# Performance work log

Measured on AMD Instinct MI355X. Metric: run time of the kernel, lower is better.

Reference implementation:

```python
import jax, jax.numpy as jnp
import numpy as np

H = 2048
EPS = 1e-12

def setup_inputs() -> dict:
    key = jax.random.key(0)
    ks = jax.random.split(key, 12)
    B, S = 2, 4096
    scale = 1.0 / np.sqrt(H)
    inp = {
        "hidden_states": jax.random.normal(ks[0], (B, S, H), dtype=jnp.float32),
        "token_type_ids": jax.random.randint(ks[1], (B, S), 0, 2, dtype=jnp.int32),
        "ln_gamma": jnp.ones((H,), jnp.float32),
        "ln_beta": jnp.zeros((H,), jnp.float32),
        "tw1": jax.random.uniform(ks[2], (H, H), jnp.float32, -scale, scale),
        "tb1": jnp.zeros((H,), jnp.float32),
        "tw2": jax.random.uniform(ks[3], (H, H), jnp.float32, -scale, scale),
        "tb2": jnp.zeros((H,), jnp.float32),
        "iw1": jax.random.uniform(ks[4], (H, H), jnp.float32, -scale, scale),
        "ib1": jnp.zeros((H,), jnp.float32),
        "iw2": jax.random.uniform(ks[5], (H, H), jnp.float32, -scale, scale),
        "ib2": jnp.zeros((H,), jnp.float32),
    }
    return inp

def _layernorm(x, g, b):
    mu = jnp.mean(x, axis=-1, keepdims=True)
    var = jnp.mean(jnp.square(x - mu), axis=-1, keepdims=True)
    return (x - mu) * jax.lax.rsqrt(var + EPS) * g + b

def _mlp(x, w1, b1, w2, b2):
    # Linear -> exact GELU -> Linear (torch nn.GELU default is erf-based)
    h = jax.nn.gelu(jnp.einsum('bsh,hk->bsk', x, w1) + b1, approximate=False)
    return jnp.einsum('bsk,kh->bsh', h, w2) + b2

def reference(hidden_states, token_type_ids, ln_gamma, ln_beta,
              tw1, tb1, tw2, tb2, iw1, ib1, iw2, ib2):
    xn = _layernorm(hidden_states, ln_gamma, ln_beta)
    text_mask = (token_type_ids == 0)[..., None]   # [B,S,1]
    image_mask = (token_type_ids == 1)[..., None]
    text_out = _mlp(xn, tw1, tb1, tw2, tb2) * text_mask
    image_out = _mlp(xn, iw1, ib1, iw2, ib2) * image_mask
    # dropout is identity in inference / p=0
    return hidden_states + text_out + image_out
```

## Files before the change

kernel.cpp:

```cpp
#include <hip/hip_runtime.h>
#include <hip/hip_bf16.h>


#define H_DIM 2048
#define FULLROWS 8192
#define TAILROWS 512
#define KSPLIT 8

typedef __attribute__((ext_vector_type(8))) short s16x8;
typedef __attribute__((ext_vector_type(4))) float f32x4;
typedef __attribute__((ext_vector_type(4))) int   i32x4;

typedef __attribute__((address_space(1))) const unsigned int gu32;
typedef __attribute__((address_space(3))) unsigned int lu32;
typedef __attribute__((address_space(3))) short lds_s;

__device__ __forceinline__ void load_lds16(const void* g, void* l) {
  __builtin_amdgcn_global_load_lds((gu32*)g, (lu32*)l, 16, 0, 0);
}

__device__ __forceinline__ s16x8 asbf(i32x4 v) {
  union { i32x4 i; s16x8 s; } u; u.i = v; return u.s;
}

__global__ __launch_bounds__(256) void partition_kernel(
    const int* __restrict__ tt, int T, int* __restrict__ ctrl,
    int* __restrict__ pos, int* __restrict__ rowid) {
  __shared__ int psum[256];
  const int tid = threadIdx.x;
  const int npt = T >> 8;
  const int base = tid * npt;
  int cnt = 0;
  for (int i = 0; i < npt; ++i) cnt += (tt[base + i] == 0);
  psum[tid] = cnt;
  __syncthreads();
  for (int off = 1; off < 256; off <<= 1) {
    int v = psum[tid];
    int add = (tid >= off) ? psum[tid - off] : 0;
    __syncthreads();
    psum[tid] = v + add;
    __syncthreads();
  }
  const int Mt = psum[255];
  const int Mt_pad = (Mt + 255) & ~255;
  int tpos = psum[tid] - cnt;
  int ipos = base - tpos;
  for (int i = 0; i < npt; ++i) {
    const int tok = base + i;
    int p;
    if (tt[tok] == 0) p = tpos++;
    else              p = Mt_pad + ipos++;
    pos[tok] = p;
    rowid[p] = tok;
  }
  const int Mi = T - Mt;
  const int Mi_pad = (Mi + 255) & ~255;
  for (int g = Mt + tid; g < Mt_pad; g += 256) rowid[g] = -1;
  for (int g = Mt_pad + Mi + tid; g < Mt_pad + Mi_pad; g += 256) rowid[g] = -1;
  for (int g = Mt_pad + Mi_pad + tid; g < FULLROWS + TAILROWS; g += 256)
    rowid[g] = -1;
  if (tid == 0) {
    ctrl[0] = Mt; ctrl[1] = Mt_pad; ctrl[2] = Mi; ctrl[3] = Mi_pad;
    ctrl[4] = Mt_pad + Mi_pad;
  }
}

__global__ __launch_bounds__(256) void pad_zero_kernel(
    const int* __restrict__ ctrl, __hip_bfloat16* __restrict__ XG) {
  const int Mt = ctrl[0], Mt_pad = ctrl[1], Mi = ctrl[2];
  const int n1 = Mt_pad - Mt;
  const int start2 = Mt_pad + Mi;
  const int b = blockIdx.x;
  int row;
  if (b < n1) row = Mt + b;
  else {
    const int b2 = b - n1;
    if (start2 + b2 >= FULLROWS + TAILROWS) return;
    row = start2 + b2;
  }
  const int4 z = {0, 0, 0, 0};
  *(int4*)(XG + (size_t)row * H_DIM + threadIdx.x * 8) = z;
}

__global__ __launch_bounds__(256) void transpose_to_bf16(
    const float* __restrict__ W, __hip_bfloat16* __restrict__ WT) {
  __shared__ float tile[32][33];
  const int bx = blockIdx.x, by = blockIdx.y;
  const int tid = threadIdx.x;
  const int r = tid >> 3, c4 = (tid & 7) * 4;
  const float4 v = *(const float4*)(W + (size_t)(by * 32 + r) * H_DIM + bx * 32 + c4);
  tile[r][c4 + 0] = v.x; tile[r][c4 + 1] = v.y;
  tile[r][c4 + 2] = v.z; tile[r][c4 + 3] = v.w;
  __syncthreads();
  union { ushort u[4]; ushort4 v4; } pk;
#pragma unroll
  for (int j = 0; j < 4; ++j) {
    __hip_bfloat16 h = __float2bfloat16(tile[c4 + j][r]);
    pk.u[j] = *(const ushort*)&h;
  }
  *(ushort4*)(WT + (size_t)(bx * 32 + r) * H_DIM + by * 32 + c4) = pk.v4;
}

__global__ __launch_bounds__(256) void ln_scatter_kernel(
    const float* __restrict__ X, const float* __restrict__ gamma,
    const float* __restrict__ beta, const int* __restrict__ pos,
    __hip_bfloat16* __restrict__ XG) {
  const int t = blockIdx.x, tid = threadIdx.x;
  const float* row = X + (size_t)t * H_DIM;
  float x[8];
  {
    float4 v0 = *(const float4*)(row + tid * 8);
    float4 v1 = *(const float4*)(row + tid * 8 + 4);
    x[0] = v0.x; x[1] = v0.y; x[2] = v0.z; x[3] = v0.w;
    x[4] = v1.x; x[5] = v1.y; x[6] = v1.z; x[7] = v1.w;
  }
  float s = 0.f, q = 0.f;
#pragma unroll
  for (int j = 0; j < 8; ++j) { s += x[j]; q += x[j] * x[j]; }
#pragma unroll
  for (int off = 32; off > 0; off >>= 1) {
    s += __shfl_down(s, off);
    q += __shfl_down(q, off);
  }
  __shared__ float ls[4], lq[4];
  if ((tid & 63) == 0) { ls[tid >> 6] = s; lq[tid >> 6] = q; }
  __syncthreads();
  const float S = ls[0] + ls[1] + ls[2] + ls[3];
  const float Q = lq[0] + lq[1] + lq[2] + lq[3];
  const float mu = S * (1.0f / H_DIM);
  const float var = Q * (1.0f / H_DIM) - mu * mu;
  const float rstd = rsqrtf(var + 1e-12f);
  const int p = pos[t];
  float4 g0 = *(const float4*)(gamma + tid * 8);
  float4 g1 = *(const float4*)(gamma + tid * 8 + 4);
  float4 b0 = *(const float4*)(beta + tid * 8);
  float4 b1 = *(const float4*)(beta + tid * 8 + 4);
  float g[8] = {g0.x, g0.y, g0.z, g0.w, g1.x, g1.y, g1.z, g1.w};
  float b[8] = {b0.x, b0.y, b0.z, b0.w, b1.x, b1.y, b1.z, b1.w};
  union { ushort u[8]; int4 v; } pk;
#pragma unroll
  for (int j = 0; j < 8; ++j) {
    float y = (x[j] - mu) * rstd * g[j] + b[j];
    __hip_bfloat16 h = __float2bfloat16(y);
    pk.u[j] = *(const ushort*)&h;
  }
  *(int4*)(XG + (size_t)p * H_DIM + tid * 8) = pk.v;
}

#define DSRD(dst, addr, OFF) \
  asm volatile("ds_read_b128 %0, %1 offset:" OFF : "=v"(dst) : "v"(addr))
#define PBAR asm volatile("s_barrier" ::: "memory")
#define SB0  __builtin_amdgcn_sched_barrier(0)
#define LGKM0 do { \
  asm volatile("s_waitcnt lgkmcnt(0)" ::: "memory"); SB0; } while (0)
#define VM0 asm volatile("s_waitcnt vmcnt(0)" ::: "memory")

__device__ __forceinline__ float gelu_exact(float z) {
  return 0.5f * z * (1.0f + erff(z * 0.70710678118654752f));
}

template <int EPI>
__global__ __launch_bounds__(512, 2) void gemmk(
    const __hip_bfloat16* __restrict__ A,
    const __hip_bfloat16* __restrict__ WTt, const __hip_bfloat16* __restrict__ WTi,
    const float* __restrict__ bt, const float* __restrict__ bi,
    const int* __restrict__ ctrl, const int* __restrict__ rowid,
    __hip_bfloat16* __restrict__ Hout,
    const float* __restrict__ resid, float* __restrict__ Out,
    float* __restrict__ pp) {
  constexpr int K = H_DIM;
  const int Mt_pad = ctrl[1];

  __shared__ __align__(16) char smem[131072];
  const unsigned sBase = (unsigned)(uintptr_t)(lds_s*)smem;

  const int tid = threadIdx.x;
  const int w = tid >> 6, l = tid & 63;
  const int bid = blockIdx.x;

  const int srow8 = l >> 3;
  const int sg = (l & 7) ^ srow8;
  const int r16 = l & 15;
  const int r4base = (l >> 4) * 4;
  const int hl = (l & 15) >> 1;
  const int gr = (((l & 1) << 2) | (l >> 4)) ^ hl;

  if (bid < 256) {
    constexpr int NT = K / 64;
    const int m0 = (bid >> 3) * 256;
    const int n0 = (bid & 7) * 256;
    const bool is_text = (m0 < Mt_pad);
    const short* Ag = (const short*)A;
    const short* Bg = (const short*)(is_text ? WTt : WTi);
    const float* bias = is_text ? bt : bi;

    const int wm = w >> 2, wn = w & 3;
    const int scol8 = sg * 8;

    auto stageA = [&](int bI, int h, int kk) {
#pragma unroll
      for (int c = 0; c < 2; ++c) {
        const short* src = Ag + (size_t)(m0 + h * 128 + c * 64 + w * 8 + srow8) * K + kk + scol8;
        load_lds16(src, smem + bI * 32768 + h * 16384 + (c * 4096 + w * 512) * 2);
      }
    };
    auto stageB = [&](int bI, int h, int kk) {
#pragma unroll
      for (int c = 0; c < 2; ++c) {
        const short* src = Bg + (size_t)(n0 + h * 128 + c * 64 + w * 8 + srow8) * K + kk + scol8;
        load_lds16(src, smem + 65536 + bI * 32768 + h * 16384 + (c * 4096 + w * 512) * 2);
      }
    };

    int off2[2];
#pragma unroll
    for (int ks = 0; ks < 2; ++ks)
      off2[ks] = r16 * 64 + (((ks * 4 + (l >> 4)) ^ (l & 7)) * 8);

    unsigned ardA[2][2], ardB[2][2];
#pragma unroll
    for (int bI = 0; bI < 2; ++bI)
#pragma unroll
      for (int ks = 0; ks < 2; ++ks) {
        ardA[bI][ks] = sBase + bI * 32768u + (unsigned)(wm * 16384 + off2[ks] * 2);
        ardB[bI][ks] = sBase + 65536u + bI * 32768u +
                       (unsigned)((wn >> 1) * 16384 + ((wn & 1) * 4096 + off2[ks]) * 2);
      }

    i32x4 a[4][2], b[4][2];
    f32x4 acc[8][4];
    const f32x4 zero = {0.f, 0.f, 0.f, 0.f};
#pragma unroll
    for (int i = 0; i < 8; ++i)
#pragma unroll
      for (int j = 0; j < 4; ++j) acc[i][j] = zero;

    auto mfmaQ = [&](int fmBase, int fnBase) {
#pragma unroll
      for (int fm = 0; fm < 4; ++fm)
#pragma unroll
        for (int fn = 0; fn < 2; ++fn)
#pragma unroll
          for (int ks = 0; ks < 2; ++ks)
            acc[fmBase + fm][fnBase + fn] = __builtin_amdgcn_mfma_f32_16x16x32_bf16(
                asbf(a[fm][ks]), asbf(b[fnBase + fn][ks]),
                acc[fmBase + fm][fnBase + fn], 0, 0, 0);
    };

#define TILE(C) do {                                                          \
    DSRD(a[0][0], ardA[C][0], "0");     DSRD(a[0][1], ardA[C][1], "0");       \
    DSRD(a[1][0], ardA[C][0], "2048");  DSRD(a[1][1], ardA[C][1], "2048");    \
    DSRD(a[2][0], ardA[C][0], "4096");  DSRD(a[2][1], ardA[C][1], "4096");    \
    DSRD(a[3][0], ardA[C][0], "6144");  DSRD(a[3][1], ardA[C][1], "6144");    \
    DSRD(b[0][0], ardB[C][0], "0");     DSRD(b[0][1], ardB[C][1], "0");       \
    DSRD(b[1][0], ardB[C][0], "2048");  DSRD(b[1][1], ardB[C][1], "2048");    \
    stageA(C ^ 1, 0, _kA);                                                    \
    PBAR; LGKM0;                                                              \
    __builtin_amdgcn_s_setprio(1); mfmaQ(0, 0); __builtin_amdgcn_s_setprio(0);\
    SB0; PBAR;                                                                \
    DSRD(b[2][0], ardB[C][0], "4096");  DSRD(b[2][1], ardB[C][1], "4096");    \
    DSRD(b[3][0], ardB[C][0], "6144");  DSRD(b[3][1], ardB[C][1], "6144");    \
    stageA(C ^ 1, 1, _kA);                                                    \
    PBAR; LGKM0;                                                              \
    __builtin_amdgcn_s_setprio(1); mfmaQ(0, 2); __builtin_amdgcn_s_setprio(0);\
    SB0; PBAR;                                                                \
    DSRD(a[0][0], ardA[C][0], "8192");  DSRD(a[0][1], ardA[C][1], "8192");    \
    DSRD(a[1][0], ardA[C][0], "10240"); DSRD(a[1][1], ardA[C][1], "10240");   \
    DSRD(a[2][0], ardA[C][0], "12288"); DSRD(a[2][1], ardA[C][1], "12288");   \
    DSRD(a[3][0], ardA[C][0], "14336"); DSRD(a[3][1], ardA[C][1], "14336");   \
    stageB(C, 0, _kB);                                                        \
    PBAR; LGKM0;                                                              \
    __builtin_amdgcn_s_setprio(1); mfmaQ(4, 2); __builtin_amdgcn_s_setprio(0);\
    SB0; PBAR;                                                                \
    stageB(C, 1, _kB);                                                        \
    asm volatile("s_waitcnt vmcnt(4)" ::: "memory");                          \
    PBAR; SB0;                                                                \
    __builtin_amdgcn_s_setprio(1); mfmaQ(4, 0); __builtin_amdgcn_s_setprio(0);\
    SB0; PBAR;                                                                \
  } while (0)

    stageA(0, 0, 0); stageA(0, 1, 0);
    stageB(0, 0, 0); stageB(0, 1, 0);
    stageB(1, 0, 64); stageB(1, 1, 64);
    asm volatile("s_waitcnt vmcnt(4)" ::: "memory");
    PBAR;

    int _kA, _kB;
    for (int t = 0; t < NT; t += 2) {
      _kA = (t + 1 < NT ? t + 1 : NT - 1) * 64;
      _kB = (t + 2 < NT ? t + 2 : NT - 1) * 64;
      TILE(0);
      _kA = (t + 2 < NT ? t + 2 : NT - 1) * 64;
      _kB = (t + 3 < NT ? t + 3 : NT - 1) * 64;
      TILE(1);
    }
#undef TILE
    asm volatile("s_waitcnt vmcnt(0) lgkmcnt(0)" ::: "memory");

    float bb[4];
#pragma unroll
    for (int fn = 0; fn < 4; ++fn) bb[fn] = bias[n0 + wn * 64 + fn * 16 + r16];
    if (EPI == 0) {
#pragma unroll
      for (int fm = 0; fm < 8; ++fm) {
        const int grow = m0 + wm * 128 + fm * 16 + r4base;
#pragma unroll
        for (int fn = 0; fn < 4; ++fn) {
          const int gcol = n0 + wn * 64 + fn * 16 + r16;
          f32x4 v = acc[fm][fn];
#pragma unroll
          for (int i = 0; i < 4; ++i)
            Hout[(size_t)(grow + i) * K + gcol] = __float2bfloat16(gelu_exact(v[i] + bb[fn]));
        }
      }
    } else {
#pragma unroll
      for (int fm = 0; fm < 8; ++fm) {
        const int grow = m0 + wm * 128 + fm * 16 + r4base;
        int rid[4];
#pragma unroll
        for (int i = 0; i < 4; ++i) rid[i] = rowid[grow + i];
#pragma unroll
        for (int fn = 0; fn < 4; ++fn) {
          const int gcol = n0 + wn * 64 + fn * 16 + r16;
          f32x4 v = acc[fm][fn];
#pragma unroll
          for (int i = 0; i < 4; ++i) {
            if (rid[i] >= 0) {
              const size_t o = (size_t)rid[i] * K + gcol;
              Out[o] = resid[o] + v[i] + bb[fn];
            }
          }
        }
      }
    }
  } else {
    const int tb = bid - 256;
    const int kp = tb & 7;
    const int n0 = ((tb >> 3) & 7) * 256;
    const int m0 = FULLROWS + (tb >> 6) * 128;
    const int kk0 = kp * 256;
    const bool is_text = (m0 < Mt_pad);
    const short* Ag = (const short*)A;
    const short* Bg = (const short*)(is_text ? WTt : WTi);

    const int wm = w >> 2, wn = w & 3;
    const int sRowAdj = sg >> 2;
    const int sKAdj = (sg & 3) * 8;

    auto stageA = [&](int bI, int kk) {
      const int mr = w * 8 + srow8;
      const short* src = Ag + (size_t)(m0 + mr * 2 + sRowAdj) * K + kk + sKAdj;
      load_lds16(src, smem + bI * 8192 + w * 1024);
    };
    auto stageB = [&](int bI, int c2, int kk) {
      const int mr = c2 * 64 + w * 8 + srow8;
      const short* src = Bg + (size_t)(n0 + mr * 2 + sRowAdj) * K + kk + sKAdj;
      load_lds16(src, smem + 16384 + bI * 16384 + c2 * 8192 + w * 1024);
    };

    unsigned ardA[2], ardB[2];
#pragma unroll
    for (int bI = 0; bI < 2; ++bI) {
      ardA[bI] = sBase + bI * 8192u + (unsigned)(wm * 4096 + hl * 128 + gr * 16);
      ardB[bI] = sBase + 16384u + bI * 16384u + (unsigned)(wn * 4096 + hl * 128 + gr * 16);
    }

    i32x4 a[4], b[4];
    f32x4 acc[4][4];
    const f32x4 zero = {0.f, 0.f, 0.f, 0.f};
#pragma unroll
    for (int i = 0; i < 4; ++i)
#pragma unroll
      for (int j = 0; j < 4; ++j) acc[i][j] = zero;

#define RD_TILE(C) do {                                                   \
    DSRD(a[0], ardA[C], "0");    DSRD(a[1], ardA[C], "1024");             \
    DSRD(a[2], ardA[C], "2048"); DSRD(a[3], ardA[C], "3072");             \
    DSRD(b[0], ardB[C], "0");    DSRD(b[1], ardB[C], "1024");             \
    DSRD(b[2], ardB[C], "2048"); DSRD(b[3], ardB[C], "3072");             \
  } while (0)

    stageA(0, kk0);
    stageB(0, 0, kk0); stageB(0, 1, kk0);
    VM0;
    PBAR;

    for (int i = 0; i < 8; ++i) {
      const int c = i & 1;
      const int kn = kk0 + (i + 1 < 8 ? i + 1 : 7) * 32;
      stageA(c ^ 1, kn);
      stageB(c ^ 1, 0, kn); stageB(c ^ 1, 1, kn);
      RD_TILE(c);
      LGKM0;
      __builtin_amdgcn_s_setprio(1);
#pragma unroll
      for (int f = 0; f < 4; ++f)
#pragma unroll
        for (int fn = 0; fn < 4; ++fn)
          acc[f][fn] = __builtin_amdgcn_mfma_f32_16x16x32_bf16(
              asbf(a[f]), asbf(b[fn]), acc[f][fn], 0, 0, 0);
      __builtin_amdgcn_s_setprio(0);
      SB0;
      VM0;
      PBAR;
    }
#undef RD_TILE
    asm volatile("s_waitcnt vmcnt(0) lgkmcnt(0)" ::: "memory");

    float* ppk = pp + (size_t)kp * TAILROWS * H_DIM;
    const int mrel = m0 - FULLROWS;
#pragma unroll
    for (int fm = 0; fm < 4; ++fm) {
      const int prow = mrel + wm * 64 + fm * 16 + r4base;
#pragma unroll
      for (int fn = 0; fn < 4; ++fn) {
        const int gcol = n0 + wn * 64 + fn * 16 + r16;
        f32x4 v = acc[fm][fn];
#pragma unroll
        for (int i = 0; i < 4; ++i)
          ppk[(size_t)(prow + i) * H_DIM + gcol] = v[i];
      }
    }
  }
}

template <int EPI>
__global__ __launch_bounds__(256) void combine_kernel(
    const float* __restrict__ pp, const float* __restrict__ bt,
    const float* __restrict__ bi, const int* __restrict__ ctrl,
    const int* __restrict__ rowid, __hip_bfloat16* __restrict__ Hout,
    const float* __restrict__ resid, float* __restrict__ Out) {
  const int u = blockIdx.x * 256 + threadIdx.x;
  const int r = u >> 9;
  const int c = (u & 511) * 4;
  const size_t off = (size_t)r * H_DIM + c;
  float4 s = *(const float4*)(pp + off);
#pragma unroll
  for (int k = 1; k < KSPLIT; ++k) {
    const float4 sk = *(const float4*)(pp + (size_t)k * TAILROWS * H_DIM + off);
    s.x += sk.x; s.y += sk.y; s.z += sk.z; s.w += sk.w;
  }
  const int grow = FULLROWS + r;
  const float* bias = (grow < ctrl[1]) ? bt : bi;
  const float4 bb = *(const float4*)(bias + c);
  if (EPI == 0) {
    union { ushort u4[4]; ushort4 v4; } pk;
    float z[4] = {s.x + bb.x, s.y + bb.y, s.z + bb.z, s.w + bb.w};
#pragma unroll
    for (int j = 0; j < 4; ++j) {
      __hip_bfloat16 h = __float2bfloat16(0.5f * z[j] * (1.0f + erff(z[j] * 0.70710678118654752f)));
      pk.u4[j] = *(const ushort*)&h;
    }
    *(ushort4*)(Hout + (size_t)grow * H_DIM + c) = pk.v4;
  } else {
    const int rid = rowid[grow];
    if (rid >= 0) {
      const size_t o = (size_t)rid * H_DIM + c;
      const float4 rv = *(const float4*)(resid + o);
      float4 ov;
      ov.x = rv.x + s.x + bb.x; ov.y = rv.y + s.y + bb.y;
      ov.z = rv.z + s.z + bb.z; ov.w = rv.w + s.w + bb.w;
      *(float4*)(Out + o) = ov;
    }
  }
}

extern "C" void kernel_launch(void* const* d_in, const int* in_sizes, int n_in,
                              void* d_out, int out_size, void* d_ws, size_t ws_size,
                              hipStream_t stream) {
  const float* hidden = (const float*)d_in[0];
  const int*   tt     = (const int*)d_in[1];
  const float* gamma  = (const float*)d_in[2];
  const float* beta   = (const float*)d_in[3];
  const float* tw1    = (const float*)d_in[4];
  const float* tb1    = (const float*)d_in[5];
  const float* tw2    = (const float*)d_in[6];
  const float* tb2    = (const float*)d_in[7];
  const float* iw1    = (const float*)d_in[8];
  const float* ib1    = (const float*)d_in[9];
  const float* iw2    = (const float*)d_in[10];
  const float* ib2    = (const float*)d_in[11];
  float* out = (float*)d_out;

  const int T = in_sizes[1];
  const int K = H_DIM;
  const int maxrows = FULLROWS + TAILROWS;

  char* ws = (char*)d_ws;
  int* ctrl  = (int*)(ws);
  int* pos   = (int*)(ws + 4096);
  int* rowid = (int*)(ws + 65536);
  const size_t WOFF = 131072;
  const size_t WSZ = (size_t)K * K * sizeof(__hip_bfloat16);
  __hip_bfloat16* wTs0 = (__hip_bfloat16*)(ws + WOFF);
  __hip_bfloat16* wTs1 = (__hip_bfloat16*)(ws + WOFF + WSZ);
  __hip_bfloat16* xg   = (__hip_bfloat16*)(ws + WOFF + 2 * WSZ);
  __hip_bfloat16* hb   = xg + (size_t)maxrows * K;
  float* pp = (float*)(hb + (size_t)maxrows * K);

  partition_kernel<<<1, 256, 0, stream>>>(tt, T, ctrl, pos, rowid);
  pad_zero_kernel<<<512, 256, 0, stream>>>(ctrl, xg);

  dim3 tg(K / 32, K / 32);
  transpose_to_bf16<<<tg, 256, 0, stream>>>(tw1, wTs0);
  transpose_to_bf16<<<tg, 256, 0, stream>>>(iw1, wTs1);

  ln_scatter_kernel<<<T, 256, 0, stream>>>(hidden, gamma, beta, pos, xg);

  gemmk<0><<<512, 512, 0, stream>>>(xg, wTs0, wTs1, tb1, ib1, ctrl, rowid,
                                    hb, nullptr, nullptr, pp);
  combine_kernel<0><<<1024, 256, 0, stream>>>(pp, tb1, ib1, ctrl, rowid,
                                              hb, nullptr, nullptr);

  transpose_to_bf16<<<tg, 256, 0, stream>>>(tw2, wTs0);
  transpose_to_bf16<<<tg, 256, 0, stream>>>(iw2, wTs1);

  gemmk<1><<<512, 512, 0, stream>>>(hb, wTs0, wTs1, tb2, ib2, ctrl, rowid,
                                    nullptr, hidden, out, pp);
  combine_kernel<1><<<1024, 256, 0, stream>>>(pp, tb2, ib2, ctrl, rowid,
                                              nullptr, hidden, out);
}
```

Measured before the change: 274.6 us.

## Unify tail split-K blocks onto the 256x256 main GEMM tile pipeline

The tail rows were handled by 256 separate split-K blocks using a smaller 128x256 tile with its own simpler pipeline. Those blocks now reuse the main 256x256 tiled, software-pipelined path over a 256-wide K slice (4 tiles), so the grid drops from 512 to 384 blocks. The aim is fewer blocks and better data reuse in the tail, since the main-loop schedule is amortized over fewer, larger tiles. In exchange, each tail block runs only 4 K-tiles, so the pipeline prologue and epilogue dominate, and the tail now has less parallelism.

Measured after the change: 272.3 us. Within noise of the previous version (-0.9%).

```diff
diff --git a/kernel.cpp b/kernel.cpp
--- a/kernel.cpp
+++ b/kernel.cpp
@@ -153,7 +153,6 @@
 #define SB0  __builtin_amdgcn_sched_barrier(0)
 #define LGKM0 do { \
   asm volatile("s_waitcnt lgkmcnt(0)" ::: "memory"); SB0; } while (0)
-#define VM0 asm volatile("s_waitcnt vmcnt(0)" ::: "memory")
 
 __device__ __forceinline__ float gelu_exact(float z) {
   return 0.5f * z * (1.0f + erff(z * 0.70710678118654752f));
@@ -178,74 +177,80 @@
   const int w = tid >> 6, l = tid & 63;
   const int bid = blockIdx.x;
 
+  int m0, n0, kbase, ntiles, kp;
+  bool partial;
+  if (bid < 256) {
+    m0 = (bid >> 3) * 256; n0 = (bid & 7) * 256;
+    kbase = 0; ntiles = 32; kp = 0; partial = false;
+  } else {
+    const int tb = bid - 256;
+    kp = tb & 7;
+    const int posn = tb >> 3;
+    n0 = (posn & 7) * 256;
+    m0 = FULLROWS + (posn >> 3) * 256;
+    kbase = kp * 256; ntiles = 4; partial = true;
+  }
+  const bool is_text = (m0 < Mt_pad);
+  const short* Ag = (const short*)A;
+  const short* Bg = (const short*)(is_text ? WTt : WTi);
+  const float* bias = is_text ? bt : bi;
+
+  const int wm = w >> 2, wn = w & 3;
   const int srow8 = l >> 3;
   const int sg = (l & 7) ^ srow8;
+  const int scol8 = sg * 8;
   const int r16 = l & 15;
   const int r4base = (l >> 4) * 4;
-  const int hl = (l & 15) >> 1;
-  const int gr = (((l & 1) << 2) | (l >> 4)) ^ hl;
-
-  if (bid < 256) {
-    constexpr int NT = K / 64;
-    const int m0 = (bid >> 3) * 256;
-    const int n0 = (bid & 7) * 256;
-    const bool is_text = (m0 < Mt_pad);
-    const short* Ag = (const short*)A;
-    const short* Bg = (const short*)(is_text ? WTt : WTi);
-    const float* bias = is_text ? bt : bi;
-
-    const int wm = w >> 2, wn = w & 3;
-    const int scol8 = sg * 8;
-
-    auto stageA = [&](int bI, int h, int kk) {
-#pragma unroll
-      for (int c = 0; c < 2; ++c) {
-        const short* src = Ag + (size_t)(m0 + h * 128 + c * 64 + w * 8 + srow8) * K + kk + scol8;
-        load_lds16(src, smem + bI * 32768 + h * 16384 + (c * 4096 + w * 512) * 2);
-      }
-    };
-    auto stageB = [&](int bI, int h, int kk) {
-#pragma unroll
-      for (int c = 0; c < 2; ++c) {
-        const short* src = Bg + (size_t)(n0 + h * 128 + c * 64 + w * 8 + srow8) * K + kk + scol8;
-        load_lds16(src, smem + 65536 + bI * 32768 + h * 16384 + (c * 4096 + w * 512) * 2);
-      }
-    };
-
-    int off2[2];
-#pragma unroll
-    for (int ks = 0; ks < 2; ++ks)
-      off2[ks] = r16 * 64 + (((ks * 4 + (l >> 4)) ^ (l & 7)) * 8);
-
-    unsigned ardA[2][2], ardB[2][2];
-#pragma unroll
-    for (int bI = 0; bI < 2; ++bI)
-#pragma unroll
-      for (int ks = 0; ks < 2; ++ks) {
-        ardA[bI][ks] = sBase + bI * 32768u + (unsigned)(wm * 16384 + off2[ks] * 2);
-        ardB[bI][ks] = sBase + 65536u + bI * 32768u +
-                       (unsigned)((wn >> 1) * 16384 + ((wn & 1) * 4096 + off2[ks]) * 2);
-      }
-
-    i32x4 a[4][2], b[4][2];
-    f32x4 acc[8][4];
-    const f32x4 zero = {0.f, 0.f, 0.f, 0.f};
-#pragma unroll
-    for (int i = 0; i < 8; ++i)
-#pragma unroll
-      for (int j = 0; j < 4; ++j) acc[i][j] = zero;
-
-    auto mfmaQ = [&](int fmBase, int fnBase) {
-#pragma unroll
-      for (int fm = 0; fm < 4; ++fm)
-#pragma unroll
-        for (int fn = 0; fn < 2; ++fn)
-#pragma unroll
-          for (int ks = 0; ks < 2; ++ks)
-            acc[fmBase + fm][fnBase + fn] = __builtin_amdgcn_mfma_f32_16x16x32_bf16(
-                asbf(a[fm][ks]), asbf(b[fnBase + fn][ks]),
-                acc[fmBase + fm][fnBase + fn], 0, 0, 0);
-    };
+
+  auto stageA = [&](int bI, int h, int kk) {
+#pragma unroll
+    for (int c = 0; c < 2; ++c) {
+      const short* src = Ag + (size_t)(m0 + h * 128 + c * 64 + w * 8 + srow8) * K + kk + scol8;
+      load_lds16(src, smem + bI * 32768 + h * 16384 + (c * 4096 + w * 512) * 2);
+    }
+  };
+  auto stageB = [&](int bI, int h, int kk) {
+#pragma unroll
+    for (int c = 0; c < 2; ++c) {
+      const short* src = Bg + (size_t)(n0 + h * 128 + c * 64 + w * 8 + srow8) * K + kk + scol8;
+      load_lds16(src, smem + 65536 + bI * 32768 + h * 16384 + (c * 4096 + w * 512) * 2);
+    }
+  };
+
+  int off2[2];
+#pragma unroll
+  for (int ks = 0; ks < 2; ++ks)
+    off2[ks] = r16 * 64 + (((ks * 4 + (l >> 4)) ^ (l & 7)) * 8);
+
+  unsigned ardA[2][2], ardB[2][2];
+#pragma unroll
+  for (int bI = 0; bI < 2; ++bI)
+#pragma unroll
+    for (int ks = 0; ks < 2; ++ks) {
+      ardA[bI][ks] = sBase + bI * 32768u + (unsigned)(wm * 16384 + off2[ks] * 2);
+      ardB[bI][ks] = sBase + 65536u + bI * 32768u +
+                     (unsigned)((wn >> 1) * 16384 + ((wn & 1) * 4096 + off2[ks]) * 2);
+    }
+
+  i32x4 a[4][2], b[4][2];
+  f32x4 acc[8][4];
+  const f32x4 zero = {0.f, 0.f, 0.f, 0.f};
+#pragma unroll
+  for (int i = 0; i < 8; ++i)
+#pragma unroll
+    for (int j = 0; j < 4; ++j) acc[i][j] = zero;
+
+  auto mfmaQ = [&](int fmBase, int fnBase) {
+#pragma unroll
+    for (int fm = 0; fm < 4; ++fm)
+#pragma unroll
+      for (int fn = 0; fn < 2; ++fn)
+#pragma unroll
+        for (int ks = 0; ks < 2; ++ks)
+          acc[fmBase + fm][fnBase + fn] = __builtin_amdgcn_mfma_f32_16x16x32_bf16(
+              asbf(a[fm][ks]), asbf(b[fnBase + fn][ks]),
+              acc[fmBase + fm][fnBase + fn], 0, 0, 0);
+  };
 
 #define TILE(C) do {                                                          \
     DSRD(a[0][0], ardA[C][0], "0");     DSRD(a[0][1], ardA[C][1], "0");       \
@@ -279,24 +284,25 @@
     SB0; PBAR;                                                                \
   } while (0)
 
-    stageA(0, 0, 0); stageA(0, 1, 0);
-    stageB(0, 0, 0); stageB(0, 1, 0);
-    stageB(1, 0, 64); stageB(1, 1, 64);
-    asm volatile("s_waitcnt vmcnt(4)" ::: "memory");
-    PBAR;
-
-    int _kA, _kB;
-    for (int t = 0; t < NT; t += 2) {
-      _kA = (t + 1 < NT ? t + 1 : NT - 1) * 64;
-      _kB = (t + 2 < NT ? t + 2 : NT - 1) * 64;
-      TILE(0);
-      _kA = (t + 2 < NT ? t + 2 : NT - 1) * 64;
-      _kB = (t + 3 < NT ? t + 3 : NT - 1) * 64;
-      TILE(1);
-    }
+  stageA(0, 0, kbase); stageA(0, 1, kbase);
+  stageB(0, 0, kbase); stageB(0, 1, kbase);
+  stageB(1, 0, kbase + 64); stageB(1, 1, kbase + 64);
+  asm volatile("s_waitcnt vmcnt(4)" ::: "memory");
+  PBAR;
+
+  int _kA, _kB;
+  for (int t = 0; t < ntiles; t += 2) {
+    _kA = kbase + (t + 1 < ntiles ? t + 1 : ntiles - 1) * 64;
+    _kB = kbase + (t + 2 < ntiles ? t + 2 : ntiles - 1) * 64;
+    TILE(0);
+    _kA = kbase + (t + 2 < ntiles ? t + 2 : ntiles - 1) * 64;
+    _kB = kbase + (t + 3 < ntiles ? t + 3 : ntiles - 1) * 64;
+    TILE(1);
+  }
 #undef TILE
-    asm volatile("s_waitcnt vmcnt(0) lgkmcnt(0)" ::: "memory");
-
+  asm volatile("s_waitcnt vmcnt(0) lgkmcnt(0)" ::: "memory");
+
+  if (!partial) {
     float bb[4];
 #pragma unroll
     for (int fn = 0; fn < 4; ++fn) bb[fn] = bias[n0 + wn * 64 + fn * 16 + r16];
@@ -335,84 +341,11 @@
       }
     }
   } else {
-    const int tb = bid - 256;
-    const int kp = tb & 7;
-    const int n0 = ((tb >> 3) & 7) * 256;
-    const int m0 = FULLROWS + (tb >> 6) * 128;
-    const int kk0 = kp * 256;
-    const bool is_text = (m0 < Mt_pad);
-    const short* Ag = (const short*)A;
-    const short* Bg = (const short*)(is_text ? WTt : WTi);
-
-    const int wm = w >> 2, wn = w & 3;
-    const int sRowAdj = sg >> 2;
-    const int sKAdj = (sg & 3) * 8;
-
-    auto stageA = [&](int bI, int kk) {
-      const int mr = w * 8 + srow8;
-      const short* src = Ag + (size_t)(m0 + mr * 2 + sRowAdj) * K + kk + sKAdj;
-      load_lds16(src, smem + bI * 8192 + w * 1024);
-    };
-    auto stageB = [&](int bI, int c2, int kk) {
-      const int mr = c2 * 64 + w * 8 + srow8;
-      const short* src = Bg + (size_t)(n0 + mr * 2 + sRowAdj) * K + kk + sKAdj;
-      load_lds16(src, smem + 16384 + bI * 16384 + c2 * 8192 + w * 1024);
-    };
-
-    unsigned ardA[2], ardB[2];
-#pragma unroll
-    for (int bI = 0; bI < 2; ++bI) {
-      ardA[bI] = sBase + bI * 8192u + (unsigned)(wm * 4096 + hl * 128 + gr * 16);
-      ardB[bI] = sBase + 16384u + bI * 16384u + (unsigned)(wn * 4096 + hl * 128 + gr * 16);
-    }
-
-    i32x4 a[4], b[4];
-    f32x4 acc[4][4];
-    const f32x4 zero = {0.f, 0.f, 0.f, 0.f};
-#pragma unroll
-    for (int i = 0; i < 4; ++i)
-#pragma unroll
-      for (int j = 0; j < 4; ++j) acc[i][j] = zero;
-
-#define RD_TILE(C) do {                                                   \
-    DSRD(a[0], ardA[C], "0");    DSRD(a[1], ardA[C], "1024");             \
-    DSRD(a[2], ardA[C], "2048"); DSRD(a[3], ardA[C], "3072");             \
-    DSRD(b[0], ardB[C], "0");    DSRD(b[1], ardB[C], "1024");             \
-    DSRD(b[2], ardB[C], "2048"); DSRD(b[3], ardB[C], "3072");             \
-  } while (0)
-
-    stageA(0, kk0);
-    stageB(0, 0, kk0); stageB(0, 1, kk0);
-    VM0;
-    PBAR;
-
-    for (int i = 0; i < 8; ++i) {
-      const int c = i & 1;
-      const int kn = kk0 + (i + 1 < 8 ? i + 1 : 7) * 32;
-      stageA(c ^ 1, kn);
-      stageB(c ^ 1, 0, kn); stageB(c ^ 1, 1, kn);
-      RD_TILE(c);
-      LGKM0;
-      __builtin_amdgcn_s_setprio(1);
-#pragma unroll
-      for (int f = 0; f < 4; ++f)
-#pragma unroll
-        for (int fn = 0; fn < 4; ++fn)
-          acc[f][fn] = __builtin_amdgcn_mfma_f32_16x16x32_bf16(
-              asbf(a[f]), asbf(b[fn]), acc[f][fn], 0, 0, 0);
-      __builtin_amdgcn_s_setprio(0);
-      SB0;
-      VM0;
-      PBAR;
-    }
-#undef RD_TILE
-    asm volatile("s_waitcnt vmcnt(0) lgkmcnt(0)" ::: "memory");
-
     float* ppk = pp + (size_t)kp * TAILROWS * H_DIM;
     const int mrel = m0 - FULLROWS;
 #pragma unroll
-    for (int fm = 0; fm < 4; ++fm) {
-      const int prow = mrel + wm * 64 + fm * 16 + r4base;
+    for (int fm = 0; fm < 8; ++fm) {
+      const int prow = mrel + wm * 128 + fm * 16 + r4base;
 #pragma unroll
       for (int fn = 0; fn < 4; ++fn) {
         const int gcol = n0 + wn * 64 + fn * 16 + r16;
@@ -508,7 +441,7 @@
 
   ln_scatter_kernel<<<T, 256, 0, stream>>>(hidden, gamma, beta, pos, xg);
 
-  gemmk<0><<<512, 512, 0, stream>>>(xg, wTs0, wTs1, tb1, ib1, ctrl, rowid,
+  gemmk<0><<<384, 512, 0, stream>>>(xg, wTs0, wTs1, tb1, ib1, ctrl, rowid,
                                     hb, nullptr, nullptr, pp);
   combine_kernel<0><<<1024, 256, 0, stream>>>(pp, tb1, ib1, ctrl, rowid,
                                               hb, nullptr, nullptr);
@@ -516,7 +449,7 @@
   transpose_to_bf16<<<tg, 256, 0, stream>>>(tw2, wTs0);
   transpose_to_bf16<<<tg, 256, 0, stream>>>(iw2, wTs1);
 
-  gemmk<1><<<512, 512, 0, stream>>>(hb, wTs0, wTs1, tb2, ib2, ctrl, rowid,
+  gemmk<1><<<384, 512, 0, stream>>>(hb, wTs0, wTs1, tb2, ib2, ctrl, rowid,
                                     nullptr, hidden, out, pp);
   combine_kernel<1><<<1024, 256, 0, stream>>>(pp, tb2, ib2, ctrl, rowid,
                                               nullptr, hidden, out);
```
